# Performance work log

Hardware: AMD Instinct MI355X
Metric: run time of the kernel (lower is better)

The kernel has to match this reference:

```python
import jax, jax.numpy as jnp
import numpy as np

LN_EPS = 1e-6

def _layernorm(x, g, b):
    mu = jnp.mean(x, axis=-1, keepdims=True)
    var = jnp.mean((x - mu) ** 2, axis=-1, keepdims=True)
    return (x - mu) / jnp.sqrt(var + LN_EPS) * g + b

def _mha(q, k, v, wq, bq, wk, bk, wv, bv, fc, fcb, ln_g, ln_b, n_head, d_k, d_v):
    # standard post-LN multi-head attention (residual + layernorm), eval mode (no dropout)
    b, lq, _ = q.shape
    bk_, lk, _ = k.shape
    residual = q
    qh = (q @ wq + bq).reshape(b, lq, n_head, d_k).transpose(0, 2, 1, 3)      # [b,h,lq,dk]
    kh = (k @ wk + bk).reshape(bk_, lk, n_head, d_k).transpose(0, 2, 1, 3)    # [bk,h,lk,dk]
    vh = (v @ wv + bv).reshape(bk_, lk, n_head, d_v).transpose(0, 2, 1, 3)    # [bk,h,lk,dv]
    attn = jax.nn.softmax(jnp.matmul(qh, kh.swapaxes(-1, -2)) / (d_k ** 0.5), axis=-1)  # [b,h,lq,lk]
    out = jnp.matmul(attn, vh)                                                # [b,h,lq,dv]
    out = out.transpose(0, 2, 1, 3).reshape(b, lq, n_head * d_v)
    pre = out
    out = _layernorm(out @ fc + fcb + residual, ln_g, ln_b)
    return out, attn, pre


def setup_inputs() -> dict:
    key = jax.random.key(0)
    ks = jax.random.split(key, 32)
    B, C, H, W = 16, 64, 32, 32
    NC, D = 5, 96  # num_classes, memory feature dim
    s = 0.05
    d = {
        'x': jax.random.normal(ks[0], (B, C, H, W), jnp.float32),
        'memory': jax.random.normal(ks[1], (NC, D), jnp.float32),
        'wb_w': jax.random.normal(ks[2], (C, NC), jnp.float32) * s,
        'wb_b': jnp.zeros((NC,), jnp.float32),
        # slf_attn: n_head=1, d_model=64, d_input_k=96, d_k=96, d_v=64
        'a1_wq': jax.random.normal(ks[3], (64, 96), jnp.float32) * s,
        'a1_bq': jnp.zeros((96,), jnp.float32),
        'a1_wk': jax.random.normal(ks[4], (96, 96), jnp.float32) * s,
        'a1_bk': jnp.zeros((96,), jnp.float32),
        'a1_wv': jax.random.normal(ks[5], (96, 64), jnp.float32) * s,
        'a1_bv': jnp.zeros((64,), jnp.float32),
        'a1_fc': jax.random.normal(ks[6], (64, 64), jnp.float32) * s,
        'a1_fcb': jnp.zeros((64,), jnp.float32),
        'a1_ln_g': jnp.ones((64,), jnp.float32),
        'a1_ln_b': jnp.zeros((64,), jnp.float32),
        # slf_attn1: n_head=4, d_model=64, d_input_k=64, d_k=64, d_v=64
        'a2_wq': jax.random.normal(ks[7], (64, 256), jnp.float32) * s,
        'a2_bq': jnp.zeros((256,), jnp.float32),
        'a2_wk': jax.random.normal(ks[8], (64, 256), jnp.float32) * s,
        'a2_bk': jnp.zeros((256,), jnp.float32),
        'a2_wv': jax.random.normal(ks[9], (64, 256), jnp.float32) * s,
        'a2_bv': jnp.zeros((256,), jnp.float32),
        'a2_fc': jax.random.normal(ks[10], (256, 64), jnp.float32) * s,
        'a2_fcb': jnp.zeros((64,), jnp.float32),
        'a2_ln_g': jnp.ones((64,), jnp.float32),
        'a2_ln_b': jnp.zeros((64,), jnp.float32),
    }
    return d


def reference(x, memory, wb_w, wb_b,
              a1_wq, a1_bq, a1_wk, a1_bk, a1_wv, a1_bv, a1_fc, a1_fcb, a1_ln_g, a1_ln_b,
              a2_wq, a2_bq, a2_wk, a2_bk, a2_wv, a2_bv, a2_fc, a2_fcb, a2_ln_g, a2_ln_b):
    b, c, H, W = x.shape
    xt = x.transpose(0, 2, 3, 1).reshape(b, H * W, c)            # [b,HW,64]
    weight = xt @ wb_w + wb_b                                    # [b,HW,5]
    weight1 = jax.nn.softmax(weight, axis=-1)                    # softmax over classes
    weight2 = jax.nn.softmax(weight.transpose(0, 2, 1), axis=-1) # [b,5,HW], softmax over HW
    class_feat1 = jnp.matmul(weight2, xt)                        # [b,5,64] class-weighted pooling
    mem = memory[None]                                           # [1,5,96]
    cf, _, _ = _mha(class_feat1, mem, mem,
                    a1_wq, a1_bq, a1_wk, a1_bk, a1_wv, a1_bv, a1_fc, a1_fcb, a1_ln_g, a1_ln_b,
                    n_head=1, d_k=96, d_v=64)                    # [b,5,64]
    cf = jnp.matmul(weight1, cf)                                 # redistribution [b,HW,64]
    cf, _, _ = _mha(cf, cf, cf,
                    a2_wq, a2_bq, a2_wk, a2_bk, a2_wv, a2_bv, a2_fc, a2_fcb, a2_ln_g, a2_ln_b,
                    n_head=4, d_k=64, d_v=64)                    # [b,HW,64]
    return cf.transpose(0, 2, 1).reshape(-1, 64, H, W)           # [b,64,H,W]
```

## Files before the change

### kernel.cpp

```cpp
#include <hip/hip_runtime.h>
#include <math.h>

typedef unsigned short ushort_t;
typedef __attribute__((ext_vector_type(8))) short short8;
typedef __attribute__((ext_vector_type(4))) float f32x4;

#define B_  16
#define HW_ 1024
#define C_  64
#define NC_ 5
#define D1_ 96
#define NH_ 4
#define DH_ 64

#define MFMA32(A,B,C) __builtin_amdgcn_mfma_f32_16x16x32_bf16(A,B,C,0,0,0)

__device__ __forceinline__ ushort_t f2bf(float f) {
    unsigned u = __float_as_uint(f);
    u = u + 0x7fffu + ((u >> 16) & 1u);
    return (ushort_t)(u >> 16);
}

__device__ __forceinline__ unsigned pack2_trunc(float lo, float hi) {
    return (__float_as_uint(hi) & 0xffff0000u) | (__float_as_uint(lo) >> 16);
}
__device__ __forceinline__ unsigned pack2_rne(float lo, float hi) {
    return ((unsigned)f2bf(hi) << 16) | (unsigned)f2bf(lo);
}
__device__ __forceinline__ float bf_lo(unsigned u) { return __uint_as_float(u << 16); }
__device__ __forceinline__ float bf_hi(unsigned u) { return __uint_as_float(u & 0xffff0000u); }

__device__ __forceinline__ void gload16(const ushort_t* g, ushort_t* l) {
    __builtin_amdgcn_global_load_lds(
        (const __attribute__((address_space(1))) unsigned int*)g,
        (__attribute__((address_space(3))) unsigned int*)l,
        16, 0, 0);
}

__global__ __launch_bounds__(256) void k0_fcT(const float* __restrict__ fc,
                                              ushort_t* __restrict__ F) {
    int c = blockIdx.x * 256 + threadIdx.x;
    int l = c & 63, s = (c >> 6) & 7, n = c >> 9;
    int col = n * 16 + (l & 15);
    int k0 = s * 32 + (l >> 4) * 8;
    union { ushort_t us[8]; uint4 u; } pk;
#pragma unroll
    for (int j = 0; j < 8; j++) pk.us[j] = f2bf(fc[(k0 + j) * 64 + col]);
    *(uint4*)(F + (size_t)c * 8) = pk.u;
}

__global__ __launch_bounds__(64) void k1_logits(const float* __restrict__ x,
                                                const float* __restrict__ wb_w,
                                                const float* __restrict__ wb_b,
                                                float* __restrict__ logitsT,
                                                float* __restrict__ w1) {
    int b = blockIdx.x >> 4;
    int hw = (blockIdx.x & 15) * 64 + threadIdx.x;
    const float* xb = x + (size_t)b * C_ * HW_;
    float acc[NC_];
#pragma unroll
    for (int j = 0; j < NC_; j++) acc[j] = wb_b[j];
#pragma unroll 8
    for (int c = 0; c < C_; c++) {
        float xv = xb[c * HW_ + hw];
#pragma unroll
        for (int j = 0; j < NC_; j++) acc[j] += xv * wb_w[c * NC_ + j];
    }
    float m = acc[0];
#pragma unroll
    for (int j = 1; j < NC_; j++) m = fmaxf(m, acc[j]);
    float e[NC_], s = 0.f;
#pragma unroll
    for (int j = 0; j < NC_; j++) { e[j] = __expf(acc[j] - m); s += e[j]; }
    float inv = 1.f / s;
    int idx = b * HW_ + hw;
#pragma unroll
    for (int j = 0; j < NC_; j++) {
        logitsT[((size_t)b * NC_ + j) * HW_ + hw] = acc[j];
        w1[(size_t)idx * NC_ + j] = e[j] * inv;
    }
}

__global__ __launch_bounds__(256) void k2b_pool(const float* __restrict__ x,
                                                const float* __restrict__ logitsT,
                                                float* __restrict__ cf1) {
    __shared__ float pl[NC_ * HW_];
    __shared__ float sinv[NC_];
    int t = threadIdx.x;
    int b = blockIdx.x >> 4, chg = blockIdx.x & 15;
    const float* lp = logitsT + (size_t)b * NC_ * HW_;
    for (int i = t * 4; i < NC_ * HW_; i += 1024)
        *(float4*)(pl + i) = *(const float4*)(lp + i);
    __syncthreads();
    int w = t >> 6, lane = t & 63;
    for (int r = w; r < NC_; r += 4) {
        float m = -1e30f;
        for (int i = lane; i < HW_; i += 64) m = fmaxf(m, pl[r * HW_ + i]);
#pragma unroll
        for (int off = 1; off < 64; off <<= 1) m = fmaxf(m, __shfl_xor(m, off, 64));
        float s = 0.f;
        for (int i = lane; i < HW_; i += 64) {
            float e = __expf(pl[r * HW_ + i] - m);
            pl[r * HW_ + i] = e;
            s += e;
        }
#pragma unroll
        for (int off = 1; off < 64; off <<= 1) s += __shfl_xor(s, off, 64);
        if (lane == 0) sinv[r] = 1.f / s;
    }
    __syncthreads();
    int ch = chg * 4 + w;
    const float* xc = x + ((size_t)b * C_ + ch) * HW_;
    float acc[NC_] = {0.f, 0.f, 0.f, 0.f, 0.f};
#pragma unroll
    for (int i = 0; i < HW_ / 64; i++) {
        int hw = i * 64 + lane;
        float xv = xc[hw];
#pragma unroll
        for (int c = 0; c < NC_; c++) acc[c] += xv * pl[c * HW_ + hw];
    }
#pragma unroll
    for (int c = 0; c < NC_; c++) {
        float a = acc[c];
#pragma unroll
        for (int off = 1; off < 64; off <<= 1) a += __shfl_xor(a, off, 64);
        if (lane == 0) cf1[((size_t)b * NC_ + c) * C_ + ch] = a * sinv[c];
    }
}

__global__ __launch_bounds__(256) void k3_mha1(const float* __restrict__ cf1,
                                               const float* __restrict__ wq, const float* __restrict__ bq,
                                               const float* __restrict__ mem,
                                               const float* __restrict__ wk, const float* __restrict__ bk,
                                               const float* __restrict__ wv, const float* __restrict__ bv,
                                               const float* __restrict__ fc, const float* __restrict__ fcb,
                                               const float* __restrict__ lng, const float* __restrict__ lnb,
                                               float* __restrict__ cfs) {
    __shared__ float cs[NC_ * C_];
    __shared__ float kh[NC_ * D1_];
    __shared__ float vh[NC_ * DH_];
    __shared__ float q[NC_ * D1_];
    __shared__ float sc[NC_ * NC_];
    __shared__ float pp[NC_ * NC_];
    __shared__ float o[NC_ * C_];
    __shared__ float z[NC_ * C_];
    __shared__ float mu[NC_], rs[NC_];
    int t = threadIdx.x, b = blockIdx.x;
    for (int i = t; i < NC_ * C_; i += 256) cs[i] = cf1[(size_t)b * NC_ * C_ + i];
    for (int idx = t; idx < NC_ * D1_; idx += 256) {
        int i = idx / D1_, k = idx % D1_;
        float a = bk[k];
        for (int d = 0; d < D1_; d++) a += mem[i * D1_ + d] * wk[d * D1_ + k];
        kh[idx] = a;
    }
    for (int idx = t; idx < NC_ * DH_; idx += 256) {
        int i = idx / DH_, dv = idx % DH_;
        float a = bv[dv];
        for (int d = 0; d < D1_; d++) a += mem[i * D1_ + d] * wv[d * DH_ + dv];
        vh[idx] = a;
    }
    __syncthreads();
    for (int idx = t; idx < NC_ * D1_; idx += 256) {
        int i = idx / D1_, k = idx % D1_;
        float a = bq[k];
        for (int c = 0; c < C_; c++) a += cs[i * C_ + c] * wq[c * D1_ + k];
        q[idx] = a;
    }
    __syncthreads();
    if (t < NC_ * NC_) {
        int i = t / NC_, j = t % NC_;
        float a = 0.f;
        for (int k = 0; k < D1_; k++) a += q[i * D1_ + k] * kh[j * D1_ + k];
        sc[t] = a * 0.1020620726159657f;
    }
    __syncthreads();
    if (t < NC_) {
        float m = sc[t * NC_];
        for (int j = 1; j < NC_; j++) m = fmaxf(m, sc[t * NC_ + j]);
        float e[NC_], s = 0.f;
        for (int j = 0; j < NC_; j++) { e[j] = __expf(sc[t * NC_ + j] - m); s += e[j]; }
        float inv = 1.f / s;
        for (int j = 0; j < NC_; j++) pp[t * NC_ + j] = e[j] * inv;
    }
    __syncthreads();
    for (int idx = t; idx < NC_ * C_; idx += 256) {
        int i = idx / C_, dv = idx % C_;
        float a = 0.f;
        for (int j = 0; j < NC_; j++) a += pp[i * NC_ + j] * vh[j * C_ + dv];
        o[idx] = a;
    }
    __syncthreads();
    for (int idx = t; idx < NC_ * C_; idx += 256) {
        int i = idx / C_, dd = idx % C_;
        float a = fcb[dd] + cs[idx];
        for (int c2 = 0; c2 < C_; c2++) a += o[i * C_ + c2] * fc[c2 * C_ + dd];
        z[idx] = a;
    }
    __syncthreads();
    if (t < NC_) {
        float s = 0.f;
        for (int d = 0; d < C_; d++) s += z[t * C_ + d];
        float mm = s / C_;
        float v = 0.f;
        for (int d = 0; d < C_; d++) { float dd2 = z[t * C_ + d] - mm; v += dd2 * dd2; }
        mu[t] = mm; rs[t] = rsqrtf(v / C_ + 1e-6f);
    }
    __syncthreads();
    for (int idx = t; idx < NC_ * C_; idx += 256) {
        int i = idx / C_, dd = idx % C_;
        cfs[(size_t)b * NC_ * C_ + idx] = (z[idx] - mu[i]) * rs[i] * lng[dd] + lnb[dd];
    }
}

__global__ __launch_bounds__(256) void k5_mfma(const float* __restrict__ w1,
                                               const float* __restrict__ cfs,
                                               const float* __restrict__ wq, const float* __restrict__ bq,
                                               const float* __restrict__ wk, const float* __restrict__ bk,
                                               const float* __restrict__ wv, const float* __restrict__ bv,
                                               ushort_t* __restrict__ Qb, ushort_t* __restrict__ Kb,
                                               ushort_t* __restrict__ Vt) {
    __shared__ ushort_t Af[64][68];
    __shared__ ushort_t Wt[256][68];
    int t = threadIdx.x;
    int which = blockIdx.y;
    int m0 = blockIdx.x * 64;
    int b = m0 >> 10, lbase = m0 & 1023;
    {
        int r = t >> 2, ks = (t & 3) * 16;
        const float* cp = cfs + (size_t)b * NC_ * C_;
        const float* w1p = w1 + (size_t)(m0 + r) * NC_;
        float v0 = w1p[0], v1 = w1p[1], v2 = w1p[2], v3 = w1p[3], v4 = w1p[4];
#pragma unroll
        for (int j = 0; j < 16; j += 2) {
            int k = ks + j;
            float e0 = v0 * cp[k]       + v1 * cp[64 + k]     + v2 * cp[128 + k]
                     + v3 * cp[192 + k] + v4 * cp[256 + k];
            float e1 = v0 * cp[k + 1]     + v1 * cp[64 + k + 1] + v2 * cp[128 + k + 1]
                     + v3 * cp[192 + k + 1] + v4 * cp[256 + k + 1];
            *(unsigned*)&Af[r][k] = pack2_rne(e0, e1);
        }
    }
    const float* W = (which == 0) ? wq : (which == 1) ? wk : wv;
    {
        int n = t;
#pragma unroll
        for (int k = 0; k < 64; k += 2) {
            *(unsigned*)&Wt[n][k] = pack2_rne(W[k * 256 + n], W[(k + 1) * 256 + n]);
        }
    }
    __syncthreads();
    int lane = t & 63, w = t >> 6;
    int l15 = lane & 15, quad = lane >> 4;
    if (which < 2) {
        const float* bias = (which == 0) ? bq : bk;
        float scale = (which == 0) ? 0.18033688011112042f : 1.0f;
        ushort_t* dst = (which == 0) ? Qb : Kb;
        short8 a0[4], a1[4];
#pragma unroll
        for (int mi = 0; mi < 4; mi++) {
            a0[mi] = *(const short8*)&Af[mi * 16 + l15][quad * 8];
            a1[mi] = *(const short8*)&Af[mi * 16 + l15][32 + quad * 8];
        }
#pragma unroll
        for (int nt = 0; nt < 4; nt++) {
            int ni = w * 4 + nt;
            short8 b0 = *(const short8*)&Wt[ni * 16 + l15][quad * 8];
            short8 b1 = *(const short8*)&Wt[ni * 16 + l15][32 + quad * 8];
            int n = ni * 16 + l15;
            float bb = bias[n];
            int h = n >> 6, dd = n & 63;
#pragma unroll
            for (int mi = 0; mi < 4; mi++) {
                f32x4 z = {0, 0, 0, 0};
                f32x4 dv4 = MFMA32(a0[mi], b0, z);
                dv4 = MFMA32(a1[mi], b1, dv4);
                size_t base = ((size_t)(b * NH_ + h) * HW_ + (lbase + mi * 16 + quad * 4)) * DH_ + dd;
#pragma unroll
                for (int r = 0; r < 4; r++)
                    dst[base + (size_t)r * DH_] = f2bf((dv4[r] + bb) * scale);
            }
        }
    } else {
        short8 a0[4], a1[4];
#pragma unroll
        for (int mt = 0; mt < 4; mt++) {
            int mi = w * 4 + mt;
            a0[mt] = *(const short8*)&Wt[mi * 16 + l15][quad * 8];
            a1[mt] = *(const short8*)&Wt[mi * 16 + l15][32 + quad * 8];
        }
#pragma unroll
        for (int nt = 0; nt < 4; nt++) {
            short8 b0 = *(const short8*)&Af[nt * 16 + l15][quad * 8];
            short8 b1 = *(const short8*)&Af[nt * 16 + l15][32 + quad * 8];
#pragma unroll
            for (int mt = 0; mt < 4; mt++) {
                int mi = w * 4 + mt;
                f32x4 z = {0, 0, 0, 0};
                f32x4 dv4 = MFMA32(a0[mt], b0, z);
                dv4 = MFMA32(a1[mt], b1, dv4);
                int h = mi >> 2;
#pragma unroll
                for (int r = 0; r < 4; r++) {
                    int nw = mi * 16 + quad * 4 + r;
                    int dv = nw & 63;
                    Vt[((size_t)(b * NH_ + h) * DH_ + dv) * HW_ + lbase + nt * 16 + l15] =
                        f2bf(dv4[r] + bv[nw]);
                }
            }
        }
    }
}

__global__ __launch_bounds__(256) void k6_attn(const ushort_t* __restrict__ Qb,
                                               const ushort_t* __restrict__ Kb,
                                               const ushort_t* __restrict__ Vt,
                                               ushort_t* __restrict__ aoP0, ushort_t* __restrict__ aoP1,
                                               float* __restrict__ sP0, float* __restrict__ sP1) {
    __shared__ ushort_t Kst[2][8][512];
    int t = threadIdx.x;
    int w = t >> 6;
    int lane = t & 63;
    int l15 = lane & 15;
    int quad = lane >> 4;
    int L = blockIdx.x;
    int bh = ((L >> 3) & 7) * 8 + (L & 7);
    int khalf = (L >> 6) & 1;
    int qt = L >> 7;
    int b = bh >> 2, h = bh & 3;
    const ushort_t* Qp = Qb + (size_t)bh * HW_ * DH_;
    const ushort_t* Kp = Kb + (size_t)bh * HW_ * DH_;
    const ushort_t* Vp = Vt + (size_t)bh * DH_ * HW_;
    int row0 = qt * 256 + w * 16;
    short8 q0[4], q1[4];
#pragma unroll
    for (int tl = 0; tl < 4; tl++) {
        const ushort_t* qp = Qp + (size_t)(row0 + tl * 64 + l15) * DH_ + quad * 8;
        q0[tl] = *(const short8*)(qp);
        q1[tl] = *(const short8*)(qp + 32);
    }
    int f0 = ((l15 >> 2) * 8) + (l15 & 3);
    int kstart = khalf * 512;
    const ushort_t* K0p = Kp + (size_t)(kstart + f0) * DH_ + quad * 8;
    const ushort_t* K1p = Kp + (size_t)(kstart + f0 + 4) * DH_ + quad * 8;
    const ushort_t* Vp0 = Vp + (size_t)(0 * 16 + l15) * HW_ + kstart + quad * 8;
    const ushort_t* Vp1 = Vp + (size_t)(1 * 16 + l15) * HW_ + kstart + quad * 8;
    const ushort_t* Vp2 = Vp + (size_t)(2 * 16 + l15) * HW_ + kstart + quad * 8;
    const ushort_t* Vp3 = Vp + (size_t)(3 * 16 + l15) * HW_ + kstart + quad * 8;
    auto stage = [&](int kt, int bb) {
        size_t koff = (size_t)kt * 32 * DH_;
        int kb32 = kt * 32;
        if (w == 0) {
            gload16(K0p + koff,      &Kst[bb][0][0]);
            gload16(K0p + koff + 32, &Kst[bb][1][0]);
        } else if (w == 1) {
            gload16(K1p + koff,      &Kst[bb][2][0]);
            gload16(K1p + koff + 32, &Kst[bb][3][0]);
        } else if (w == 2) {
            gload16(Vp0 + kb32, &Kst[bb][4][0]);
            gload16(Vp1 + kb32, &Kst[bb][5][0]);
        } else {
            gload16(Vp2 + kb32, &Kst[bb][6][0]);
            gload16(Vp3 + kb32, &Kst[bb][7][0]);
        }
    };
    const short ONE = (short)0x3F80;
    short8 ones = {ONE, ONE, ONE, ONE, ONE, ONE, ONE, ONE};
    f32x4 o0[4], o1[4], o2[4], o3[4], oS[4];
#pragma unroll
    for (int tl = 0; tl < 4; tl++) {
        o0[tl] = (f32x4){0,0,0,0}; o1[tl] = (f32x4){0,0,0,0};
        o2[tl] = (f32x4){0,0,0,0}; o3[tl] = (f32x4){0,0,0,0};
        oS[tl] = (f32x4){0,0,0,0};
    }
    stage(0, 0);
    for (int kt = 0; kt < 16; kt++) {
        int bb = kt & 1;
        __syncthreads();
        if (kt < 15) stage(kt + 1, bb ^ 1);
        const ushort_t* S = &Kst[bb][0][0];
        short8 ka0 = *(const short8*)(S + 0 * 512 + lane * 8);
        short8 ka1 = *(const short8*)(S + 1 * 512 + lane * 8);
        short8 kb0 = *(const short8*)(S + 2 * 512 + lane * 8);
        short8 kb1 = *(const short8*)(S + 3 * 512 + lane * 8);
        short8 v0  = *(const short8*)(S + 4 * 512 + lane * 8);
        short8 v1  = *(const short8*)(S + 5 * 512 + lane * 8);
        short8 v2  = *(const short8*)(S + 6 * 512 + lane * 8);
        short8 v3  = *(const short8*)(S + 7 * 512 + lane * 8);
        f32x4 z = {0,0,0,0};
#pragma unroll
        for (int tl = 0; tl < 4; tl++) {
            f32x4 s0 = MFMA32(ka0, q0[tl], z);  s0 = MFMA32(ka1, q1[tl], s0);
            f32x4 s1 = MFMA32(kb0, q0[tl], z);  s1 = MFMA32(kb1, q1[tl], s1);
            float p0 = exp2f(s0[0]), p1 = exp2f(s0[1]), p2 = exp2f(s0[2]), p3 = exp2f(s0[3]);
            float p4 = exp2f(s1[0]), p5 = exp2f(s1[1]), p6 = exp2f(s1[2]), p7 = exp2f(s1[3]);
            union { short8 v; unsigned u[4]; } pf;
            pf.u[0] = pack2_trunc(p0, p1);  pf.u[1] = pack2_trunc(p2, p3);
            pf.u[2] = pack2_trunc(p4, p5);  pf.u[3] = pack2_trunc(p6, p7);
            o0[tl] = MFMA32(v0, pf.v, o0[tl]);
            o1[tl] = MFMA32(v1, pf.v, o1[tl]);
            o2[tl] = MFMA32(v2, pf.v, o2[tl]);
            o3[tl] = MFMA32(v3, pf.v, o3[tl]);
            oS[tl] = MFMA32(ones, pf.v, oS[tl]);
        }
    }
    ushort_t* aoP = khalf ? aoP1 : aoP0;
    float* sP = khalf ? sP1 : sP0;
#pragma unroll
    for (int tl = 0; tl < 4; tl++) {
        int rowg = row0 + tl * 64 + l15;
        ushort_t* aop = aoP + ((size_t)(b * HW_ + rowg)) * 256 + h * 64 + quad * 4;
        uint2 u;
        u.x = pack2_trunc(o0[tl][0], o0[tl][1]); u.y = pack2_trunc(o0[tl][2], o0[tl][3]);
        *(uint2*)(aop + 0) = u;
        u.x = pack2_trunc(o1[tl][0], o1[tl][1]); u.y = pack2_trunc(o1[tl][2], o1[tl][3]);
        *(uint2*)(aop + 16) = u;
        u.x = pack2_trunc(o2[tl][0], o2[tl][1]); u.y = pack2_trunc(o2[tl][2], o2[tl][3]);
        *(uint2*)(aop + 32) = u;
        u.x = pack2_trunc(o3[tl][0], o3[tl][1]); u.y = pack2_trunc(o3[tl][2], o3[tl][3]);
        *(uint2*)(aop + 48) = u;
        if (quad == 0)
            sP[(size_t)(b * HW_ + rowg) * NH_ + h] = oS[tl][0];
    }
}

__global__ __launch_bounds__(256) void k7_final(const ushort_t* __restrict__ aoP0,
                                                const ushort_t* __restrict__ aoP1,
                                                const float* __restrict__ sP0,
                                                const float* __restrict__ sP1,
                                                const float* __restrict__ w1,
                                                const float* __restrict__ cfs,
                                                const ushort_t* __restrict__ F,
                                                const float* __restrict__ fcb,
                                                const float* __restrict__ lng, const float* __restrict__ lnb,
                                                float* __restrict__ out) {
    __shared__ ushort_t Afr[512 * 8];
    __shared__ float rinv[64];
    __shared__ float T[16][68];
    __shared__ float To[64 * 17];
    int t = threadIdx.x, w = t >> 6, lane = t & 63;
    int m0 = blockIdx.x * 16, b = m0 >> 10;
    if (t < 64) {
        int row = t >> 2, hh = t & 3;
        float s = sP0[(size_t)(m0 + row) * NH_ + hh] + sP1[(size_t)(m0 + row) * NH_ + hh];
        rinv[t] = 1.f / s;
    }
    __syncthreads();
#pragma unroll
    for (int cc = t; cc < 512; cc += 256) {
        int s = cc >> 6, l = cc & 63;
        int row = l & 15, col0 = s * 32 + (l >> 4) * 8;
        int hh = col0 >> 6;
        size_t base = (size_t)(m0 + row) * 256 + col0;
        uint4 a = *(const uint4*)(aoP0 + base);
        uint4 c4 = *(const uint4*)(aoP1 + base);
        float r = rinv[row * 4 + hh];
        uint4 pk;
        pk.x = pack2_trunc((bf_lo(a.x) + bf_lo(c4.x)) * r, (bf_hi(a.x) + bf_hi(c4.x)) * r);
        pk.y = pack2_trunc((bf_lo(a.y) + bf_lo(c4.y)) * r, (bf_hi(a.y) + bf_hi(c4.y)) * r);
        pk.z = pack2_trunc((bf_lo(a.z) + bf_lo(c4.z)) * r, (bf_hi(a.z) + bf_hi(c4.z)) * r);
        pk.w = pack2_trunc((bf_lo(a.w) + bf_lo(c4.w)) * r, (bf_hi(a.w) + bf_hi(c4.w)) * r);
        *(uint4*)&Afr[(size_t)cc * 8] = pk;
    }
    __syncthreads();
    f32x4 acc = {0, 0, 0, 0};
#pragma unroll
    for (int s = 0; s < 8; s++) {
        short8 a = *(const short8*)&Afr[(s * 64 + lane) * 8];
        short8 bf8 = *(const short8*)(F + ((size_t)(w * 8 + s) * 64 + lane) * 8);
        acc = MFMA32(a, bf8, acc);
    }
    {
        int l15 = lane & 15, quad = lane >> 4;
#pragma unroll
        for (int r = 0; r < 4; r++) T[quad * 4 + r][w * 16 + l15] = acc[r];
    }
    __syncthreads();
    int d = lane;
    float g = lng[d], be = lnb[d], bias = fcb[d];
    const float* cp = cfs + (size_t)b * NC_ * C_;
#pragma unroll
    for (int j = 0; j < 4; j++) {
        int row = w * 4 + j;
        const float* w1p = w1 + (size_t)(m0 + row) * NC_;
        float a = bias + T[row][d];
#pragma unroll
        for (int c = 0; c < NC_; c++) a += w1p[c] * cp[c * 64 + d];
        float s1 = a, s2 = a * a;
#pragma unroll
        for (int off = 1; off < 64; off <<= 1) {
            s1 += __shfl_xor(s1, off, 64);
            s2 += __shfl_xor(s2, off, 64);
        }
        float mu = s1 * (1.f / 64.f);
        float var = s2 * (1.f / 64.f) - mu * mu;
        float rstd = rsqrtf(var + 1e-6f);
        To[d * 17 + row] = (a - mu) * rstd * g + be;
    }
    __syncthreads();
    int ch = t >> 2, part = t & 3;
    int hw0 = m0 & 1023;
    float4 v = {To[ch * 17 + part * 4 + 0], To[ch * 17 + part * 4 + 1],
                To[ch * 17 + part * 4 + 2], To[ch * 17 + part * 4 + 3]};
    *(float4*)&out[((size_t)b * 64 + ch) * 1024 + hw0 + part * 4] = v;
}

extern "C" void kernel_launch(void* const* d_in, const int* in_sizes, int n_in,
                              void* d_out, int out_size, void* d_ws, size_t ws_size,
                              hipStream_t stream) {
    const float* x      = (const float*)d_in[0];
    const float* memory = (const float*)d_in[1];
    const float* wb_w   = (const float*)d_in[2];
    const float* wb_b   = (const float*)d_in[3];
    const float* a1_wq  = (const float*)d_in[4];
    const float* a1_bq  = (const float*)d_in[5];
    const float* a1_wk  = (const float*)d_in[6];
    const float* a1_bk  = (const float*)d_in[7];
    const float* a1_wv  = (const float*)d_in[8];
    const float* a1_bv  = (const float*)d_in[9];
    const float* a1_fc  = (const float*)d_in[10];
    const float* a1_fcb = (const float*)d_in[11];
    const float* a1_ln_g = (const float*)d_in[12];
    const float* a1_ln_b = (const float*)d_in[13];
    const float* a2_wq  = (const float*)d_in[14];
    const float* a2_bq  = (const float*)d_in[15];
    const float* a2_wk  = (const float*)d_in[16];
    const float* a2_bk  = (const float*)d_in[17];
    const float* a2_wv  = (const float*)d_in[18];
    const float* a2_bv  = (const float*)d_in[19];
    const float* a2_fc  = (const float*)d_in[20];
    const float* a2_fcb = (const float*)d_in[21];
    const float* a2_ln_g = (const float*)d_in[22];
    const float* a2_ln_b = (const float*)d_in[23];

    float* ws = (float*)d_ws;
    float* logitsT = ws;
    float* w1  = logitsT + 81920;
    float* cf1 = w1 + 81920;
    float* cfs = cf1 + 5120;
    float* sP0 = cfs + 5120;
    float* sP1 = sP0 + 65536;
    ushort_t* aoP0 = (ushort_t*)(sP1 + 65536);
    ushort_t* aoP1 = aoP0 + 4194304;
    ushort_t* Qb = aoP1 + 4194304;
    ushort_t* Kb = Qb + 4194304;
    ushort_t* Vt = Kb + 4194304;
    ushort_t* F  = Vt + 4194304;

    k0_fcT<<<8, 256, 0, stream>>>(a2_fc, F);
    k1_logits<<<256, 64, 0, stream>>>(x, wb_w, wb_b, logitsT, w1);
    k2b_pool<<<256, 256, 0, stream>>>(x, logitsT, cf1);
    k3_mha1<<<16, 256, 0, stream>>>(cf1, a1_wq, a1_bq, memory, a1_wk, a1_bk,
                                    a1_wv, a1_bv, a1_fc, a1_fcb,
                                    a1_ln_g, a1_ln_b, cfs);
    k5_mfma<<<dim3(256, 3), 256, 0, stream>>>(w1, cfs, a2_wq, a2_bq, a2_wk, a2_bk,
                                              a2_wv, a2_bv, Qb, Kb, Vt);
    k6_attn<<<512, 256, 0, stream>>>(Qb, Kb, Vt, aoP0, aoP1, sP0, sP1);
    k7_final<<<1024, 256, 0, stream>>>(aoP0, aoP1, sP0, sP1, w1, cfs, F, a2_fcb,
                                       a2_ln_g, a2_ln_b, (float*)d_out);
}
```

Measured before the change: 191.5 us.

## Stage QKV projection outputs in LDS for coalesced stores, deepen attention K/V staging

The QKV projection kernel now writes its MFMA results into a shared-memory tile (reusing the weight buffer after a barrier) and then emits 16-byte coalesced global stores, replacing scattered 2-byte stores for Q, K and the transposed V. The separate fc-weight conversion kernel is folded into the projection kernel's tail, removing one launch. The attention kernel stages two 32-key tiles per barrier by doubling the LDS buffer, halving the number of synchronisations. This costs more LDS per block, which may reduce occupancy in the attention kernel.

```diff
diff --git a/kernel.cpp b/kernel.cpp
--- a/kernel.cpp
+++ b/kernel.cpp
@@ -35,18 +35,6 @@
         (const __attribute__((address_space(1))) unsigned int*)g,
         (__attribute__((address_space(3))) unsigned int*)l,
         16, 0, 0);
-}
-
-__global__ __launch_bounds__(256) void k0_fcT(const float* __restrict__ fc,
-                                              ushort_t* __restrict__ F) {
-    int c = blockIdx.x * 256 + threadIdx.x;
-    int l = c & 63, s = (c >> 6) & 7, n = c >> 9;
-    int col = n * 16 + (l & 15);
-    int k0 = s * 32 + (l >> 4) * 8;
-    union { ushort_t us[8]; uint4 u; } pk;
-#pragma unroll
-    for (int j = 0; j < 8; j++) pk.us[j] = f2bf(fc[(k0 + j) * 64 + col]);
-    *(uint4*)(F + (size_t)c * 8) = pk.u;
 }
 
 __global__ __launch_bounds__(64) void k1_logits(const float* __restrict__ x,
@@ -217,8 +205,9 @@
                                                const float* __restrict__ wq, const float* __restrict__ bq,
                                                const float* __restrict__ wk, const float* __restrict__ bk,
                                                const float* __restrict__ wv, const float* __restrict__ bv,
+                                               const float* __restrict__ fc2,
                                                ushort_t* __restrict__ Qb, ushort_t* __restrict__ Kb,
-                                               ushort_t* __restrict__ Vt) {
+                                               ushort_t* __restrict__ Vt, ushort_t* __restrict__ F) {
     __shared__ ushort_t Af[64][68];
     __shared__ ushort_t Wt[256][68];
     int t = threadIdx.x;
@@ -255,7 +244,8 @@
         const float* bias = (which == 0) ? bq : bk;
         float scale = (which == 0) ? 0.18033688011112042f : 1.0f;
         ushort_t* dst = (which == 0) ? Qb : Kb;
-        short8 a0[4], a1[4];
+        short8 a0[4], a1[4], b0[4], b1[4];
+        float bias4[4];
 #pragma unroll
         for (int mi = 0; mi < 4; mi++) {
             a0[mi] = *(const short8*)&Af[mi * 16 + l15][quad * 8];
@@ -264,24 +254,44 @@
 #pragma unroll
         for (int nt = 0; nt < 4; nt++) {
             int ni = w * 4 + nt;
-            short8 b0 = *(const short8*)&Wt[ni * 16 + l15][quad * 8];
-            short8 b1 = *(const short8*)&Wt[ni * 16 + l15][32 + quad * 8];
-            int n = ni * 16 + l15;
-            float bb = bias[n];
-            int h = n >> 6, dd = n & 63;
+            b0[nt] = *(const short8*)&Wt[ni * 16 + l15][quad * 8];
+            b1[nt] = *(const short8*)&Wt[ni * 16 + l15][32 + quad * 8];
+            bias4[nt] = bias[ni * 16 + l15];
+        }
+        __syncthreads();
+        ushort_t* Qt = &Wt[0][0];
+#pragma unroll
+        for (int nt = 0; nt < 4; nt++) {
+            int ncol = (w * 4 + nt) * 16 + l15;
 #pragma unroll
             for (int mi = 0; mi < 4; mi++) {
                 f32x4 z = {0, 0, 0, 0};
-                f32x4 dv4 = MFMA32(a0[mi], b0, z);
-                dv4 = MFMA32(a1[mi], b1, dv4);
-                size_t base = ((size_t)(b * NH_ + h) * HW_ + (lbase + mi * 16 + quad * 4)) * DH_ + dd;
-#pragma unroll
-                for (int r = 0; r < 4; r++)
-                    dst[base + (size_t)r * DH_] = f2bf((dv4[r] + bb) * scale);
+                f32x4 dv4 = MFMA32(a0[mi], b0[nt], z);
+                dv4 = MFMA32(a1[mi], b1[nt], dv4);
+#pragma unroll
+                for (int r = 0; r < 4; r++) {
+                    int l = mi * 16 + quad * 4 + r;
+                    Qt[l * 264 + ncol] = f2bf((dv4[r] + bias4[nt]) * scale);
+                }
             }
         }
+        __syncthreads();
+        int l = t >> 2, hq = t & 3;
+        uint4 v0q = *(const uint4*)&Qt[l * 264 + hq * 64 + 0];
+        uint4 v1q = *(const uint4*)&Qt[l * 264 + hq * 64 + 8];
+        uint4 v2q = *(const uint4*)&Qt[l * 264 + hq * 64 + 16];
+        uint4 v3q = *(const uint4*)&Qt[l * 264 + hq * 64 + 24];
+        uint4 v4q = *(const uint4*)&Qt[l * 264 + hq * 64 + 32];
+        uint4 v5q = *(const uint4*)&Qt[l * 264 + hq * 64 + 40];
+        uint4 v6q = *(const uint4*)&Qt[l * 264 + hq * 64 + 48];
+        uint4 v7q = *(const uint4*)&Qt[l * 264 + hq * 64 + 56];
+        ushort_t* gp = dst + ((size_t)(b * NH_ + hq) * HW_ + lbase + l) * DH_;
+        *(uint4*)(gp + 0)  = v0q;  *(uint4*)(gp + 8)  = v1q;
+        *(uint4*)(gp + 16) = v2q;  *(uint4*)(gp + 24) = v3q;
+        *(uint4*)(gp + 32) = v4q;  *(uint4*)(gp + 40) = v5q;
+        *(uint4*)(gp + 48) = v6q;  *(uint4*)(gp + 56) = v7q;
     } else {
-        short8 a0[4], a1[4];
+        short8 a0[4], a1[4], b0[4], b1[4];
 #pragma unroll
         for (int mt = 0; mt < 4; mt++) {
             int mi = w * 4 + mt;
@@ -290,24 +300,47 @@
         }
 #pragma unroll
         for (int nt = 0; nt < 4; nt++) {
-            short8 b0 = *(const short8*)&Af[nt * 16 + l15][quad * 8];
-            short8 b1 = *(const short8*)&Af[nt * 16 + l15][32 + quad * 8];
+            b0[nt] = *(const short8*)&Af[nt * 16 + l15][quad * 8];
+            b1[nt] = *(const short8*)&Af[nt * 16 + l15][32 + quad * 8];
+        }
+        __syncthreads();
+        ushort_t* Vtile = &Wt[0][0];
+#pragma unroll
+        for (int nt = 0; nt < 4; nt++) {
 #pragma unroll
             for (int mt = 0; mt < 4; mt++) {
                 int mi = w * 4 + mt;
                 f32x4 z = {0, 0, 0, 0};
-                f32x4 dv4 = MFMA32(a0[mt], b0, z);
-                dv4 = MFMA32(a1[mt], b1, dv4);
-                int h = mi >> 2;
+                f32x4 dv4 = MFMA32(a0[mt], b0[nt], z);
+                dv4 = MFMA32(a1[mt], b1[nt], dv4);
 #pragma unroll
                 for (int r = 0; r < 4; r++) {
                     int nw = mi * 16 + quad * 4 + r;
-                    int dv = nw & 63;
-                    Vt[((size_t)(b * NH_ + h) * DH_ + dv) * HW_ + lbase + nt * 16 + l15] =
-                        f2bf(dv4[r] + bv[nw]);
+                    Vtile[nw * 68 + nt * 16 + l15] = f2bf(dv4[r] + bv[nw]);
                 }
             }
         }
+        __syncthreads();
+        int nw = t, h = nw >> 6, dv = nw & 63;
+        uint2 u[16];
+#pragma unroll
+        for (int j = 0; j < 16; j++) u[j] = *(const uint2*)&Vtile[nw * 68 + j * 4];
+        ushort_t* gp = Vt + ((size_t)(b * NH_ + h) * DH_ + dv) * HW_ + lbase;
+#pragma unroll
+        for (int j = 0; j < 8; j++) {
+            uint4 vv = {u[2 * j].x, u[2 * j].y, u[2 * j + 1].x, u[2 * j + 1].y};
+            *(uint4*)(gp + j * 8) = vv;
+        }
+    }
+    if (which == 0 && t < 8) {
+        int c = blockIdx.x * 8 + t;
+        int l = c & 63, s = (c >> 6) & 7, n = c >> 9;
+        int col = n * 16 + (l & 15);
+        int k0 = s * 32 + (l >> 4) * 8;
+        union { ushort_t us[8]; uint4 u; } pk;
+#pragma unroll
+        for (int j = 0; j < 8; j++) pk.us[j] = f2bf(fc2[(k0 + j) * 64 + col]);
+        *(uint4*)(F + (size_t)c * 8) = pk.u;
     }
 }
 
@@ -316,7 +349,7 @@
                                                const ushort_t* __restrict__ Vt,
                                                ushort_t* __restrict__ aoP0, ushort_t* __restrict__ aoP1,
                                                float* __restrict__ sP0, float* __restrict__ sP1) {
-    __shared__ ushort_t Kst[2][8][512];
+    __shared__ ushort_t Kst[2][16][512];
     int t = threadIdx.x;
     int w = t >> 6;
     int lane = t & 63;
@@ -349,18 +382,19 @@
     auto stage = [&](int kt, int bb) {
         size_t koff = (size_t)kt * 32 * DH_;
         int kb32 = kt * 32;
+        int half = (kt & 1) * 8;
         if (w == 0) {
-            gload16(K0p + koff,      &Kst[bb][0][0]);
-            gload16(K0p + koff + 32, &Kst[bb][1][0]);
+            gload16(K0p + koff,      &Kst[bb][half + 0][0]);
+            gload16(K0p + koff + 32, &Kst[bb][half + 1][0]);
         } else if (w == 1) {
-            gload16(K1p + koff,      &Kst[bb][2][0]);
-            gload16(K1p + koff + 32, &Kst[bb][3][0]);
+            gload16(K1p + koff,      &Kst[bb][half + 2][0]);
+            gload16(K1p + koff + 32, &Kst[bb][half + 3][0]);
         } else if (w == 2) {
-            gload16(Vp0 + kb32, &Kst[bb][4][0]);
-            gload16(Vp1 + kb32, &Kst[bb][5][0]);
+            gload16(Vp0 + kb32, &Kst[bb][half + 4][0]);
+            gload16(Vp1 + kb32, &Kst[bb][half + 5][0]);
         } else {
-            gload16(Vp2 + kb32, &Kst[bb][6][0]);
-            gload16(Vp3 + kb32, &Kst[bb][7][0]);
+            gload16(Vp2 + kb32, &Kst[bb][half + 6][0]);
+            gload16(Vp3 + kb32, &Kst[bb][half + 7][0]);
         }
     };
     const short ONE = (short)0x3F80;
@@ -373,34 +407,38 @@
         oS[tl] = (f32x4){0,0,0,0};
     }
     stage(0, 0);
-    for (int kt = 0; kt < 16; kt++) {
-        int bb = kt & 1;
+    stage(1, 0);
+    for (int p = 0; p < 8; p++) {
+        int bb = p & 1;
         __syncthreads();
-        if (kt < 15) stage(kt + 1, bb ^ 1);
-        const ushort_t* S = &Kst[bb][0][0];
-        short8 ka0 = *(const short8*)(S + 0 * 512 + lane * 8);
-        short8 ka1 = *(const short8*)(S + 1 * 512 + lane * 8);
-        short8 kb0 = *(const short8*)(S + 2 * 512 + lane * 8);
-        short8 kb1 = *(const short8*)(S + 3 * 512 + lane * 8);
-        short8 v0  = *(const short8*)(S + 4 * 512 + lane * 8);
-        short8 v1  = *(const short8*)(S + 5 * 512 + lane * 8);
-        short8 v2  = *(const short8*)(S + 6 * 512 + lane * 8);
-        short8 v3  = *(const short8*)(S + 7 * 512 + lane * 8);
-        f32x4 z = {0,0,0,0};
-#pragma unroll
-        for (int tl = 0; tl < 4; tl++) {
-            f32x4 s0 = MFMA32(ka0, q0[tl], z);  s0 = MFMA32(ka1, q1[tl], s0);
-            f32x4 s1 = MFMA32(kb0, q0[tl], z);  s1 = MFMA32(kb1, q1[tl], s1);
-            float p0 = exp2f(s0[0]), p1 = exp2f(s0[1]), p2 = exp2f(s0[2]), p3 = exp2f(s0[3]);
-            float p4 = exp2f(s1[0]), p5 = exp2f(s1[1]), p6 = exp2f(s1[2]), p7 = exp2f(s1[3]);
-            union { short8 v; unsigned u[4]; } pf;
-            pf.u[0] = pack2_trunc(p0, p1);  pf.u[1] = pack2_trunc(p2, p3);
-            pf.u[2] = pack2_trunc(p4, p5);  pf.u[3] = pack2_trunc(p6, p7);
-            o0[tl] = MFMA32(v0, pf.v, o0[tl]);
-            o1[tl] = MFMA32(v1, pf.v, o1[tl]);
-            o2[tl] = MFMA32(v2, pf.v, o2[tl]);
-            o3[tl] = MFMA32(v3, pf.v, o3[tl]);
-            oS[tl] = MFMA32(ones, pf.v, oS[tl]);
+        if (p < 7) { stage(2 * p + 2, bb ^ 1); stage(2 * p + 3, bb ^ 1); }
+#pragma unroll
+        for (int half = 0; half < 2; half++) {
+            const ushort_t* S = &Kst[bb][half * 8][0];
+            short8 ka0 = *(const short8*)(S + 0 * 512 + lane * 8);
+            short8 ka1 = *(const short8*)(S + 1 * 512 + lane * 8);
+            short8 kb0 = *(const short8*)(S + 2 * 512 + lane * 8);
+            short8 kb1 = *(const short8*)(S + 3 * 512 + lane * 8);
+            short8 v0  = *(const short8*)(S + 4 * 512 + lane * 8);
+            short8 v1  = *(const short8*)(S + 5 * 512 + lane * 8);
+            short8 v2  = *(const short8*)(S + 6 * 512 + lane * 8);
+            short8 v3  = *(const short8*)(S + 7 * 512 + lane * 8);
+            f32x4 z = {0,0,0,0};
+#pragma unroll
+            for (int tl = 0; tl < 4; tl++) {
+                f32x4 s0 = MFMA32(ka0, q0[tl], z);  s0 = MFMA32(ka1, q1[tl], s0);
+                f32x4 s1 = MFMA32(kb0, q0[tl], z);  s1 = MFMA32(kb1, q1[tl], s1);
+                float p0 = exp2f(s0[0]), p1 = exp2f(s0[1]), p2 = exp2f(s0[2]), p3 = exp2f(s0[3]);
+                float p4 = exp2f(s1[0]), p5 = exp2f(s1[1]), p6 = exp2f(s1[2]), p7 = exp2f(s1[3]);
+                union { short8 v; unsigned u[4]; } pf;
+                pf.u[0] = pack2_trunc(p0, p1);  pf.u[1] = pack2_trunc(p2, p3);
+                pf.u[2] = pack2_trunc(p4, p5);  pf.u[3] = pack2_trunc(p6, p7);
+                o0[tl] = MFMA32(v0, pf.v, o0[tl]);
+                o1[tl] = MFMA32(v1, pf.v, o1[tl]);
+                o2[tl] = MFMA32(v2, pf.v, o2[tl]);
+                o3[tl] = MFMA32(v3, pf.v, o3[tl]);
+                oS[tl] = MFMA32(ones, pf.v, oS[tl]);
+            }
         }
     }
     ushort_t* aoP = khalf ? aoP1 : aoP0;
@@ -546,14 +584,13 @@
     ushort_t* Vt = Kb + 4194304;
     ushort_t* F  = Vt + 4194304;
 
-    k0_fcT<<<8, 256, 0, stream>>>(a2_fc, F);
     k1_logits<<<256, 64, 0, stream>>>(x, wb_w, wb_b, logitsT, w1);
     k2b_pool<<<256, 256, 0, stream>>>(x, logitsT, cf1);
     k3_mha1<<<16, 256, 0, stream>>>(cf1, a1_wq, a1_bq, memory, a1_wk, a1_bk,
                                     a1_wv, a1_bv, a1_fc, a1_fcb,
                                     a1_ln_g, a1_ln_b, cfs);
     k5_mfma<<<dim3(256, 3), 256, 0, stream>>>(w1, cfs, a2_wq, a2_bq, a2_wk, a2_bk,
-                                              a2_wv, a2_bv, Qb, Kb, Vt);
+                                              a2_wv, a2_bv, a2_fc, Qb, Kb, Vt, F);
     k6_attn<<<512, 256, 0, stream>>>(Qb, Kb, Vt, aoP0, aoP1, sP0, sP1);
     k7_final<<<1024, 256, 0, stream>>>(aoP0, aoP1, sP0, sP1, w1, cfs, F, a2_fcb,
                                        a2_ln_g, a2_ln_b, (float*)d_out);
```

Result: slower. 197.2 us (+3.0%).
